# Optimization experiments

Hardware: AMD Instinct MI355X
Metric: run time of the kernel (lower is better)

The kernel has to match this reference:

```python
import math
import jax, jax.numpy as jnp
import numpy as np

B, L, D, H = 4, 1024, 1024, 16
HD = D // H  # head_dim = 64


def rel_pos_embed(seq_len: int, dim: int, padding_idx: int = 0) -> jnp.ndarray:
    """RelativeSinusoidalPositionalEmbedding for seq_len > origin_shift case:
    table regenerated with num_embeddings = 2*seq_len, origin_shift = seq_len,
    positions = arange(-L, L) + L selects the full table. Returns [2L, dim]."""
    num = 2 * seq_len
    half = dim // 2
    scale = math.log(10000.0) / (half - 1)
    freq = np.exp(np.arange(half, dtype=np.float32) * -scale)
    pos = np.arange(-num // 2, num // 2, dtype=np.float32)
    emb = pos[:, None] * freq[None, :]                      # [2L, half]
    emb = np.concatenate([np.sin(emb), np.cos(emb)], axis=1).astype(np.float32)
    emb[padding_idx] = 0.0
    return jnp.asarray(emb)


def _shift(BD):
    """Transformer-XL shift: [b,n,L,2L] -> [b,n,L,L] aligning relative positions."""
    b, n, l, _ = BD.shape
    zero_pad = jnp.zeros((b, n, l, 1), BD.dtype)
    BD = jnp.concatenate([BD, zero_pad], axis=-1).reshape(b, n, -1, l)  # [b,n,2L+1,L]
    BD = BD[:, :, : 2 * l].reshape(b, n, l, -1)                          # [b,n,L,2L]
    return BD[..., l:]                                                    # [b,n,L,L]


def setup_inputs() -> dict:
    key = jax.random.key(0)
    k0, k1, k2, k3 = jax.random.split(key, 4)
    x = jax.random.normal(k0, (B, L, D), jnp.float32)
    Wqv = jax.random.normal(k1, (D, 2 * D), jnp.float32) * (1.0 / math.sqrt(D))
    r_r_bias = jax.random.normal(k2, (H, HD), jnp.float32) * 0.1
    r_w_bias = jax.random.normal(k3, (H, HD), jnp.float32) * 0.1
    mask = jnp.ones((B, L), jnp.int32)
    return {"x": x, "Wqv": Wqv, "r_r_bias": r_r_bias, "r_w_bias": r_w_bias, "mask": mask}


def reference(x, Wqv, r_r_bias, r_w_bias, mask):
    b, l, d = x.shape
    pos = rel_pos_embed(l, HD)                               # [2L, HD] (detached buffer)
    qv = x @ Wqv                                             # [b, L, 2D]
    q, v = jnp.split(qv, 2, axis=-1)
    q = q.reshape(b, l, H, HD).transpose(0, 2, 1, 3)         # [b, H, L, HD]
    v = v.reshape(b, l, H, HD).transpose(0, 2, 1, 3)
    k = x.reshape(b, l, H, HD).transpose(0, 2, 1, 3)         # k_as_x=True: k is x reshaped

    rw_head_q = q + r_r_bias[None, :, None, :]
    AC = jnp.einsum('bnqd,bnkd->bnqk', rw_head_q, k)         # [b,H,L,L]
    D_ = jnp.einsum('nd,ld->nl', r_w_bias, pos)[None, :, None, :]  # [1,H,1,2L]
    B_ = jnp.einsum('bnqd,ld->bnql', q, pos)                 # [b,H,L,2L]
    BD = _shift(B_ + D_)                                     # [b,H,L,L]

    attn = AC + BD
    attn = jnp.where(mask[:, None, None, :] == 0, -jnp.inf, attn)
    attn = jax.nn.softmax(attn, axis=-1)                     # dropout is identity (eval)
    out = jnp.einsum('bnqk,bnkd->bnqd', attn, v)
    return out.transpose(0, 2, 1, 3).reshape(b, l, d)
```

## Files before the change

### kernel.cpp

```cpp
#include <hip/hip_runtime.h>
#include <hip/hip_bf16.h>
#include <math.h>


typedef __attribute__((ext_vector_type(8))) short short8;
typedef __attribute__((ext_vector_type(4))) short short4v;
typedef __attribute__((ext_vector_type(4))) float f32x4;

#define MFMA16(a,b,c) __builtin_amdgcn_mfma_f32_16x16x32_bf16(a,b,c,0,0,0)

__device__ __forceinline__ short f2bf(float f) {
  union { float f; unsigned int u; } v; v.f = f;
  unsigned int u = v.u;
  u += 0x7FFFu + ((u >> 16) & 1u);
  return (short)(u >> 16);
}
__device__ __forceinline__ float bf2f(short h) {
  union { unsigned int u; float f; } v;
  v.u = ((unsigned int)(unsigned short)h) << 16;
  return v.f;
}
__device__ __forceinline__ void glds16(const short* g, short* l) {
  __builtin_amdgcn_global_load_lds(
      (const __attribute__((address_space(1))) void*)g,
      (__attribute__((address_space(3))) void*)l, 16, 0, 0);
}

__global__ __launch_bounds__(256) void k_trig(float* __restrict__ T) {
  int idx = blockIdx.x * 256 + threadIdx.x;
  int l = idx >> 6, c = idx & 63, cc = c & 31;
  float fr = (float)exp(-(double)cc * 0.2971077539347156);
  double ang = (double)l * (double)fr;
  T[idx] = (float)((c < 32) ? sin(ang) : cos(ang));
}

__global__ __launch_bounds__(256) void k_split_x(const float* __restrict__ x,
    short* __restrict__ xh, short* __restrict__ xl) {
  int i = blockIdx.x * 256 + threadIdx.x;
  f32x4 v = ((const f32x4*)x)[i];
  short4v h, l;
#pragma unroll
  for (int c = 0; c < 4; ++c) {
    short hb = f2bf(v[c]);
    h[c] = hb;
    l[c] = f2bf(v[c] - bf2f(hb));
  }
  ((short4v*)xh)[i] = h;
  ((short4v*)xl)[i] = l;
}

__global__ __launch_bounds__(256) void k_wt(const float* __restrict__ W,
    short* __restrict__ wth, short* __restrict__ wtl) {
  __shared__ __align__(16) float tile[64*65];
  int n0 = blockIdx.x * 64, k0 = blockIdx.y * 64;
  int tid = threadIdx.x;
#pragma unroll
  for (int i = 0; i < 16; ++i) {
    int e = tid + i*256, r = e >> 6, c = e & 63;
    tile[r*65 + c] = W[(k0 + r)*2048 + n0 + c];
  }
  __syncthreads();
#pragma unroll
  for (int i = 0; i < 16; ++i) {
    int e = tid + i*256, r = e >> 6, c = e & 63;
    float v = tile[c*65 + r];
    short hb = f2bf(v);
    wth[(n0 + r)*1024 + k0 + c] = hb;
    wtl[(n0 + r)*1024 + k0 + c] = f2bf(v - bf2f(hb));
  }
}

__global__ __launch_bounds__(256) void k_gemm(
    const short* __restrict__ xh, const short* __restrict__ xl,
    const short* __restrict__ wth, const short* __restrict__ wtl,
    float* __restrict__ qf, short* __restrict__ vbt) {
  __shared__ __align__(16) short Ah[128*32], Al[128*32], Bh[128*32], Bl[128*32];
  int tid = threadIdx.x;
  int m0 = blockIdx.x * 128, n0 = blockIdx.y * 128;
  int lane = tid & 63, w = tid >> 6;
  int wm = w >> 1, wn = w & 1;
  int g = lane >> 4, lr = lane & 15;
  f32x4 acc[4][4] = {};
  for (int kt = 0; kt < 32; ++kt) {
    int k0 = kt * 32;
#pragma unroll
    for (int p = 0; p < 2; ++p) {
      int e = p*256 + tid;
      int r = e >> 2, c8 = (e & 3) * 8, e8 = e * 8;
      glds16(&xh [(m0+r)*1024 + k0 + c8], &Ah[e8]);
      glds16(&xl [(m0+r)*1024 + k0 + c8], &Al[e8]);
      glds16(&wth[(n0+r)*1024 + k0 + c8], &Bh[e8]);
      glds16(&wtl[(n0+r)*1024 + k0 + c8], &Bl[e8]);
    }
    __syncthreads();
    short8 ah[4], al[4], bh[4], bl[4];
#pragma unroll
    for (int mf = 0; mf < 4; ++mf) {
      int row = wm*64 + mf*16 + lr;
      ah[mf] = *(short8*)&Ah[row*32 + g*8];
      al[mf] = *(short8*)&Al[row*32 + g*8];
    }
#pragma unroll
    for (int nf = 0; nf < 4; ++nf) {
      int row = wn*64 + nf*16 + lr;
      bh[nf] = *(short8*)&Bh[row*32 + g*8];
      bl[nf] = *(short8*)&Bl[row*32 + g*8];
    }
    __builtin_amdgcn_s_setprio(1);
#pragma unroll
    for (int mf = 0; mf < 4; ++mf)
#pragma unroll
      for (int nf = 0; nf < 4; ++nf) {
        acc[mf][nf] = MFMA16(ah[mf], bh[nf], acc[mf][nf]);
        acc[mf][nf] = MFMA16(al[mf], bh[nf], acc[mf][nf]);
        acc[mf][nf] = MFMA16(ah[mf], bl[nf], acc[mf][nf]);
      }
    __builtin_amdgcn_s_setprio(0);
    __syncthreads();
  }
#pragma unroll
  for (int mf = 0; mf < 4; ++mf)
#pragma unroll
    for (int nf = 0; nf < 4; ++nf) {
      int row0 = m0 + wm*64 + mf*16 + g*4;
      int col  = n0 + wn*64 + nf*16 + lr;
      if (col < 1024) {
#pragma unroll
        for (int ri = 0; ri < 4; ++ri)
          qf[(row0 + ri)*1024 + col] = acc[mf][nf][ri];
      } else {
        int c2 = col - 1024, h = c2 >> 6, d = c2 & 63;
        int b = row0 >> 10, l0 = row0 & 1023;
        short4v pk;
#pragma unroll
        for (int ri = 0; ri < 4; ++ri) pk[ri] = f2bf(acc[mf][nf][ri]);
        *(short4v*)&vbt[((b*16 + h)*64 + d)*1024 + l0] = pk;
      }
    }
}

__global__ __launch_bounds__(256) void k_qcat(const float* __restrict__ qf,
    const float* __restrict__ rrb, const float* __restrict__ rwb,
    const float* __restrict__ T, short* __restrict__ qch, short* __restrict__ qcl) {
  int row = blockIdx.x * 4 + (threadIdx.x >> 6);
  int lane = threadIdx.x & 63;
  int b = row >> 14, h = (row >> 10) & 15, l = row & 1023;
  float q  = qf[(b*1024 + l)*1024 + h*64 + lane];
  float qa = q + rrb[h*64 + lane];
  float qb = q + rwb[h*64 + lane];
  int c = lane & 31;
  float qs = __shfl(qb, c, 64);
  float qc = __shfl(qb, c + 32, 64);
  float ts = T[l*64 + c];
  float tc = T[l*64 + c + 32];
  float v2 = (lane < 32) ? (qs*tc + qc*ts) : (qc*tc - qs*ts);
  short ha = f2bf(qa), h2 = f2bf(v2);
  qch[row*128 + lane]      = ha;
  qcl[row*128 + lane]      = f2bf(qa - bf2f(ha));
  qch[row*128 + 64 + lane] = h2;
  qcl[row*128 + 64 + lane] = f2bf(v2 - bf2f(h2));
}

__global__ __launch_bounds__(256) void k_kcat(const float* __restrict__ x,
    const float* __restrict__ T, short* __restrict__ kch, short* __restrict__ kcl) {
  int row = blockIdx.x * 4 + (threadIdx.x >> 6);
  int lane = threadIdx.x & 63;
  int b = row >> 14, h = (row >> 10) & 15, k = row & 1023;
  float xv = x[(b*1024 + k)*1024 + h*64 + lane];
  float tv = T[k*64 + lane];
  short hx = f2bf(xv), ht = f2bf(tv);
  int sw = k & 7;
  int c0 = lane, c1 = 64 + lane;
  int p0 = ((((c0 >> 3) ^ sw) << 3) | (c0 & 7));
  int p1 = ((((c1 >> 3) ^ sw) << 3) | (c1 & 7));
  kch[row*128 + p0] = hx;
  kcl[row*128 + p0] = f2bf(xv - bf2f(hx));
  kch[row*128 + p1] = ht;
  kcl[row*128 + p1] = f2bf(tv - bf2f(ht));
}

#define NKT 32
#define PLDW 40
__global__ __launch_bounds__(256, 2) void k_attn(
    const short* __restrict__ qch, const short* __restrict__ qcl,
    const short* __restrict__ kch, const short* __restrict__ kcl,
    const short* __restrict__ vbt, float* __restrict__ out) {
  __shared__ __align__(16) short Kh[2][32*128], Kl[2][32*128];
  __shared__ __align__(16) short Pl[4][2][16*PLDW];
  int tid = threadIdx.x, lane = tid & 63, w = tid >> 6;
  int g = lane >> 4, lr = lane & 15;
  int id = blockIdx.x;
  int s = id >> 3, xcd = id & 7;
  int bh = xcd*8 + (s & 7), qt = s >> 3;
  int q0 = qt * 128;
  short8 qh[2][4], ql[2][4];
#pragma unroll
  for (int m = 0; m < 2; ++m) {
    int qrow = bh*1024 + q0 + w*32 + m*16 + lr;
#pragma unroll
    for (int kc = 0; kc < 4; ++kc) {
      qh[m][kc] = *(const short8*)&qch[qrow*128 + kc*32 + g*8];
      ql[m][kc] = *(const short8*)&qcl[qrow*128 + kc*32 + g*8];
    }
  }
  f32x4 o[2][5] = {};
  float m_run[2][4];
#pragma unroll
  for (int m = 0; m < 2; ++m)
#pragma unroll
    for (int r = 0; r < 4; ++r) m_run[m][r] = -1e30f;
  short8 onesv;
#pragma unroll
  for (int i = 0; i < 8; ++i) onesv[i] = (short)0x3F80;
#pragma unroll
  for (int p = 0; p < 2; ++p) {
    int e8 = (p*256 + tid) * 8;
    glds16(&kch[(bh*1024)*128 + e8], &Kh[0][e8]);
    glds16(&kcl[(bh*1024)*128 + e8], &Kl[0][e8]);
  }
  __syncthreads();
  for (int kt = 0; kt < NKT; ++kt) {
    int cur = kt & 1;
    short8 vb[4];
#pragma unroll
    for (int df = 0; df < 4; ++df)
      vb[df] = *(const short8*)&vbt[(bh*64 + df*16 + lr)*1024 + kt*32 + g*8];
    if (kt + 1 < NKT) {
      int off = (bh*1024 + (kt+1)*32)*128;
#pragma unroll
      for (int p = 0; p < 2; ++p) {
        int e8 = (p*256 + tid) * 8;
        glds16(&kch[off + e8], &Kh[cur^1][e8]);
        glds16(&kcl[off + e8], &Kl[cur^1][e8]);
      }
    }
    f32x4 sacc[2][2] = {};
    __builtin_amdgcn_s_setprio(1);
#pragma unroll
    for (int kc = 0; kc < 4; ++kc)
#pragma unroll
      for (int nf = 0; nf < 2; ++nf) {
        int boff = (nf*16 + lr)*256 + ((((kc<<2) + g) ^ (lr & 7)) << 4);
        short8 kbh = *(short8*)((char*)&Kh[cur][0] + boff);
        short8 kbl = *(short8*)((char*)&Kl[cur][0] + boff);
#pragma unroll
        for (int m = 0; m < 2; ++m) {
          sacc[m][nf] = MFMA16(qh[m][kc], kbh, sacc[m][nf]);
          sacc[m][nf] = MFMA16(ql[m][kc], kbh, sacc[m][nf]);
          sacc[m][nf] = MFMA16(qh[m][kc], kbl, sacc[m][nf]);
        }
      }
    __builtin_amdgcn_s_setprio(0);
    float mt[2][4];
#pragma unroll
    for (int m = 0; m < 2; ++m)
#pragma unroll
      for (int r = 0; r < 4; ++r)
        mt[m][r] = fmaxf(sacc[m][0][r], sacc[m][1][r]);
#pragma unroll
    for (int off = 1; off < 16; off <<= 1)
#pragma unroll
      for (int m = 0; m < 2; ++m)
#pragma unroll
        for (int r = 0; r < 4; ++r)
          mt[m][r] = fmaxf(mt[m][r], __shfl_xor(mt[m][r], off, 64));
    float dmax = mt[0][0] - m_run[0][0];
#pragma unroll
    for (int m = 0; m < 2; ++m)
#pragma unroll
      for (int r = 0; r < 4; ++r)
        dmax = fmaxf(dmax, mt[m][r] - m_run[m][r]);
    if (!__all(dmax <= 8.0f)) {
#pragma unroll
      for (int m = 0; m < 2; ++m)
#pragma unroll
        for (int r = 0; r < 4; ++r) {
          float mn = fmaxf(m_run[m][r], mt[m][r]);
          float sc = __expf(m_run[m][r] - mn);
          m_run[m][r] = mn;
#pragma unroll
          for (int df = 0; df < 5; ++df) o[m][df][r] *= sc;
        }
    }
#pragma unroll
    for (int m = 0; m < 2; ++m)
#pragma unroll
      for (int nf = 0; nf < 2; ++nf)
#pragma unroll
        for (int r = 0; r < 4; ++r) {
          float p = __expf(sacc[m][nf][r] - m_run[m][r]);
          Pl[w][m][(g*4 + r)*PLDW + nf*16 + lr] = f2bf(p);
        }
    __builtin_amdgcn_s_setprio(1);
#pragma unroll
    for (int m = 0; m < 2; ++m) {
      short8 pa = *(short8*)&Pl[w][m][lr*PLDW + g*8];
#pragma unroll
      for (int df = 0; df < 4; ++df)
        o[m][df] = MFMA16(pa, vb[df], o[m][df]);
      o[m][4] = MFMA16(pa, onesv, o[m][4]);
    }
    __builtin_amdgcn_s_setprio(0);
    __syncthreads();
  }
  int b = bh >> 4, h = bh & 15;
#pragma unroll
  for (int m = 0; m < 2; ++m)
#pragma unroll
    for (int df = 0; df < 4; ++df)
#pragma unroll
      for (int r = 0; r < 4; ++r) {
        int qa = q0 + w*32 + m*16 + g*4 + r;
        out[(b*1024 + qa)*1024 + h*64 + df*16 + lr] = o[m][df][r] / o[m][4][r];
      }
}

extern "C" void kernel_launch(void* const* d_in, const int* in_sizes, int n_in,
                              void* d_out, int out_size, void* d_ws, size_t ws_size,
                              hipStream_t stream) {
  const float* x   = (const float*)d_in[0];
  const float* Wqv = (const float*)d_in[1];
  const float* rrb = (const float*)d_in[2];
  const float* rwb = (const float*)d_in[3];
  float* out = (float*)d_out;
  char* ws = (char*)d_ws;
  const size_t MB = 1u << 20;
  float* T   = (float*)(ws);
  short* vbt = (short*)(ws + 1*MB);
  short* qch = (short*)(ws + 9*MB);
  short* qcl = (short*)(ws + 25*MB);
  short* kch = (short*)(ws + 41*MB);
  short* kcl = (short*)(ws + 57*MB);
  short* xh  = (short*)(ws + 41*MB);
  short* xl  = (short*)(ws + 49*MB);
  short* wth = (short*)(ws + 57*MB);
  short* wtl = (short*)(ws + 61*MB);
  float* qf  = (float*)d_out;

  hipLaunchKernelGGL(k_trig,   dim3(256),      dim3(256), 0, stream, T);
  hipLaunchKernelGGL(k_split_x,dim3(4096),     dim3(256), 0, stream, x, xh, xl);
  hipLaunchKernelGGL(k_wt,     dim3(32, 16),   dim3(256), 0, stream, Wqv, wth, wtl);
  hipLaunchKernelGGL(k_gemm,   dim3(32, 16),   dim3(256), 0, stream, xh, xl, wth, wtl, qf, vbt);
  hipLaunchKernelGGL(k_qcat,   dim3(16384),    dim3(256), 0, stream, qf, rrb, rwb, T, qch, qcl);
  hipLaunchKernelGGL(k_kcat,   dim3(16384),    dim3(256), 0, stream, x, T, kch, kcl);
  hipLaunchKernelGGL(k_attn,   dim3(512),      dim3(256), 0, stream, qch, qcl, kch, kcl, vbt, out);
}
```

Before: 249.2 us.

## Split attention over key halves with combine kernel, double-buffer GEMM, trim V-block MFMAs

The attention kernel now splits the key range into two halves across twice as many blocks (1024 instead of 512) and targets four blocks per CU via launch bounds. A new combine kernel merges the unnormalized partial outputs using saved row max and sum. The goal is to fill more CUs and hide latency, at the cost of extra partial-output traffic and one more launch. Separately, the QV GEMM double-buffers its LDS tiles and drops the low-weight MFMA for V columns, which only need bf16 output. The online-softmax rescale check is also made cheaper: the cross-lane max reduction now runs only when some lane exceeds its threshold.

```diff
diff --git a/kernel.cpp b/kernel.cpp
--- a/kernel.cpp
+++ b/kernel.cpp
@@ -74,48 +74,71 @@
     const short* __restrict__ xh, const short* __restrict__ xl,
     const short* __restrict__ wth, const short* __restrict__ wtl,
     float* __restrict__ qf, short* __restrict__ vbt) {
-  __shared__ __align__(16) short Ah[128*32], Al[128*32], Bh[128*32], Bl[128*32];
+  __shared__ __align__(16) short Ah[2][128*32], Al[2][128*32],
+                                 Bh[2][128*32], Bl[2][128*32];
   int tid = threadIdx.x;
   int m0 = blockIdx.x * 128, n0 = blockIdx.y * 128;
+  bool vblock = (n0 >= 1024);
   int lane = tid & 63, w = tid >> 6;
   int wm = w >> 1, wn = w & 1;
   int g = lane >> 4, lr = lane & 15;
   f32x4 acc[4][4] = {};
+#define GSTAGE(kt, buf) do { \
+    int k0_ = (kt)*32; \
+    _Pragma("unroll") \
+    for (int p = 0; p < 2; ++p) { \
+      int e = p*256 + tid; \
+      int r = e >> 2, c8 = (e & 3)*8, e8 = e*8; \
+      glds16(&xh [(m0+r)*1024 + k0_ + c8], &Ah[buf][e8]); \
+      glds16(&xl [(m0+r)*1024 + k0_ + c8], &Al[buf][e8]); \
+      glds16(&wth[(n0+r)*1024 + k0_ + c8], &Bh[buf][e8]); \
+      if (!vblock) glds16(&wtl[(n0+r)*1024 + k0_ + c8], &Bl[buf][e8]); \
+    } \
+  } while (0)
+  GSTAGE(0, 0);
+  __syncthreads();
   for (int kt = 0; kt < 32; ++kt) {
-    int k0 = kt * 32;
-#pragma unroll
-    for (int p = 0; p < 2; ++p) {
-      int e = p*256 + tid;
-      int r = e >> 2, c8 = (e & 3) * 8, e8 = e * 8;
-      glds16(&xh [(m0+r)*1024 + k0 + c8], &Ah[e8]);
-      glds16(&xl [(m0+r)*1024 + k0 + c8], &Al[e8]);
-      glds16(&wth[(n0+r)*1024 + k0 + c8], &Bh[e8]);
-      glds16(&wtl[(n0+r)*1024 + k0 + c8], &Bl[e8]);
-    }
-    __syncthreads();
+    int cur = kt & 1;
+    if (kt + 1 < 32) GSTAGE(kt + 1, cur ^ 1);
     short8 ah[4], al[4], bh[4], bl[4];
 #pragma unroll
     for (int mf = 0; mf < 4; ++mf) {
       int row = wm*64 + mf*16 + lr;
-      ah[mf] = *(short8*)&Ah[row*32 + g*8];
-      al[mf] = *(short8*)&Al[row*32 + g*8];
+      ah[mf] = *(short8*)&Ah[cur][row*32 + g*8];
+      al[mf] = *(short8*)&Al[cur][row*32 + g*8];
     }
 #pragma unroll
     for (int nf = 0; nf < 4; ++nf) {
       int row = wn*64 + nf*16 + lr;
-      bh[nf] = *(short8*)&Bh[row*32 + g*8];
-      bl[nf] = *(short8*)&Bl[row*32 + g*8];
-    }
-    __builtin_amdgcn_s_setprio(1);
-#pragma unroll
-    for (int mf = 0; mf < 4; ++mf)
+      bh[nf] = *(short8*)&Bh[cur][row*32 + g*8];
+    }
+    if (!vblock) {
 #pragma unroll
       for (int nf = 0; nf < 4; ++nf) {
-        acc[mf][nf] = MFMA16(ah[mf], bh[nf], acc[mf][nf]);
-        acc[mf][nf] = MFMA16(al[mf], bh[nf], acc[mf][nf]);
-        acc[mf][nf] = MFMA16(ah[mf], bl[nf], acc[mf][nf]);
-      }
-    __builtin_amdgcn_s_setprio(0);
+        int row = wn*64 + nf*16 + lr;
+        bl[nf] = *(short8*)&Bl[cur][row*32 + g*8];
+      }
+      __builtin_amdgcn_s_setprio(1);
+#pragma unroll
+      for (int mf = 0; mf < 4; ++mf)
+#pragma unroll
+        for (int nf = 0; nf < 4; ++nf) {
+          acc[mf][nf] = MFMA16(ah[mf], bh[nf], acc[mf][nf]);
+          acc[mf][nf] = MFMA16(al[mf], bh[nf], acc[mf][nf]);
+          acc[mf][nf] = MFMA16(ah[mf], bl[nf], acc[mf][nf]);
+        }
+      __builtin_amdgcn_s_setprio(0);
+    } else {
+      __builtin_amdgcn_s_setprio(1);
+#pragma unroll
+      for (int mf = 0; mf < 4; ++mf)
+#pragma unroll
+        for (int nf = 0; nf < 4; ++nf) {
+          acc[mf][nf] = MFMA16(ah[mf], bh[nf], acc[mf][nf]);
+          acc[mf][nf] = MFMA16(al[mf], bh[nf], acc[mf][nf]);
+        }
+      __builtin_amdgcn_s_setprio(0);
+    }
     __syncthreads();
   }
 #pragma unroll
@@ -179,19 +202,20 @@
   kcl[row*128 + p1] = f2bf(tv - bf2f(ht));
 }
 
-#define NKT 32
+#define NKT 16
 #define PLDW 40
-__global__ __launch_bounds__(256, 2) void k_attn(
+__global__ __launch_bounds__(256, 4) void k_attn(
     const short* __restrict__ qch, const short* __restrict__ qcl,
     const short* __restrict__ kch, const short* __restrict__ kcl,
-    const short* __restrict__ vbt, float* __restrict__ out) {
+    const short* __restrict__ vbt, float* __restrict__ p0,
+    float* __restrict__ p1, float* __restrict__ ml) {
   __shared__ __align__(16) short Kh[2][32*128], Kl[2][32*128];
   __shared__ __align__(16) short Pl[4][2][16*PLDW];
   int tid = threadIdx.x, lane = tid & 63, w = tid >> 6;
   int g = lane >> 4, lr = lane & 15;
   int id = blockIdx.x;
   int s = id >> 3, xcd = id & 7;
-  int bh = xcd*8 + (s & 7), qt = s >> 3;
+  int bh = xcd*8 + (s & 7), qt = (s >> 3) & 7, sp = s >> 6;
   int q0 = qt * 128;
   short8 qh[2][4], ql[2][4];
 #pragma unroll
@@ -212,21 +236,25 @@
   short8 onesv;
 #pragma unroll
   for (int i = 0; i < 8; ++i) onesv[i] = (short)0x3F80;
-#pragma unroll
-  for (int p = 0; p < 2; ++p) {
-    int e8 = (p*256 + tid) * 8;
-    glds16(&kch[(bh*1024)*128 + e8], &Kh[0][e8]);
-    glds16(&kcl[(bh*1024)*128 + e8], &Kl[0][e8]);
+  {
+    int kbase = (bh*1024 + sp*512)*128;
+#pragma unroll
+    for (int p = 0; p < 2; ++p) {
+      int e8 = (p*256 + tid) * 8;
+      glds16(&kch[kbase + e8], &Kh[0][e8]);
+      glds16(&kcl[kbase + e8], &Kl[0][e8]);
+    }
   }
   __syncthreads();
-  for (int kt = 0; kt < NKT; ++kt) {
-    int cur = kt & 1;
+  for (int t = 0; t < NKT; ++t) {
+    int cur = t & 1;
+    int ktg = sp*16 + t;
     short8 vb[4];
 #pragma unroll
     for (int df = 0; df < 4; ++df)
-      vb[df] = *(const short8*)&vbt[(bh*64 + df*16 + lr)*1024 + kt*32 + g*8];
-    if (kt + 1 < NKT) {
-      int off = (bh*1024 + (kt+1)*32)*128;
+      vb[df] = *(const short8*)&vbt[(bh*64 + df*16 + lr)*1024 + ktg*32 + g*8];
+    if (t + 1 < NKT) {
+      int off = (bh*1024 + (ktg+1)*32)*128;
 #pragma unroll
       for (int p = 0; p < 2; ++p) {
         int e8 = (p*256 + tid) * 8;
@@ -251,31 +279,28 @@
         }
       }
     __builtin_amdgcn_s_setprio(0);
-    float mt[2][4];
+    float pm[2][4];
+    int trig = 0;
 #pragma unroll
     for (int m = 0; m < 2; ++m)
 #pragma unroll
-      for (int r = 0; r < 4; ++r)
-        mt[m][r] = fmaxf(sacc[m][0][r], sacc[m][1][r]);
-#pragma unroll
-    for (int off = 1; off < 16; off <<= 1)
+      for (int r = 0; r < 4; ++r) {
+        pm[m][r] = fmaxf(sacc[m][0][r], sacc[m][1][r]);
+        trig |= (pm[m][r] > m_run[m][r] + 8.0f);
+      }
+    if (__any(trig)) {
+#pragma unroll
+      for (int off = 1; off < 16; off <<= 1)
+#pragma unroll
+        for (int m = 0; m < 2; ++m)
+#pragma unroll
+          for (int r = 0; r < 4; ++r)
+            pm[m][r] = fmaxf(pm[m][r], __shfl_xor(pm[m][r], off, 64));
 #pragma unroll
       for (int m = 0; m < 2; ++m)
 #pragma unroll
-        for (int r = 0; r < 4; ++r)
-          mt[m][r] = fmaxf(mt[m][r], __shfl_xor(mt[m][r], off, 64));
-    float dmax = mt[0][0] - m_run[0][0];
-#pragma unroll
-    for (int m = 0; m < 2; ++m)
-#pragma unroll
-      for (int r = 0; r < 4; ++r)
-        dmax = fmaxf(dmax, mt[m][r] - m_run[m][r]);
-    if (!__all(dmax <= 8.0f)) {
-#pragma unroll
-      for (int m = 0; m < 2; ++m)
-#pragma unroll
         for (int r = 0; r < 4; ++r) {
-          float mn = fmaxf(m_run[m][r], mt[m][r]);
+          float mn = fmaxf(m_run[m][r], pm[m][r]);
           float sc = __expf(m_run[m][r] - mn);
           m_run[m][r] = mn;
 #pragma unroll
@@ -303,6 +328,7 @@
     __builtin_amdgcn_s_setprio(0);
     __syncthreads();
   }
+  float* pp = sp ? p1 : p0;
   int b = bh >> 4, h = bh & 15;
 #pragma unroll
   for (int m = 0; m < 2; ++m)
@@ -311,8 +337,37 @@
 #pragma unroll
       for (int r = 0; r < 4; ++r) {
         int qa = q0 + w*32 + m*16 + g*4 + r;
-        out[(b*1024 + qa)*1024 + h*64 + df*16 + lr] = o[m][df][r] / o[m][4][r];
-      }
+        pp[(b*1024 + qa)*1024 + h*64 + df*16 + lr] = o[m][df][r];
+      }
+  if (lr == 0) {
+#pragma unroll
+    for (int m = 0; m < 2; ++m)
+#pragma unroll
+      for (int r = 0; r < 4; ++r) {
+        int qa = q0 + w*32 + m*16 + g*4 + r;
+        int mlr = (sp*65536 + bh*1024 + qa)*2;
+        ml[mlr]     = m_run[m][r];
+        ml[mlr + 1] = o[m][4][r];
+      }
+  }
+}
+
+__global__ __launch_bounds__(256) void k_comb(const float* p0,
+    const float* __restrict__ p1, const float* __restrict__ ml, float* outp) {
+  int idx = (blockIdx.x*256 + threadIdx.x) * 4;
+  int b = idx >> 20, qa = (idx >> 10) & 1023, h = (idx >> 6) & 15;
+  int row = (b*16 + h)*1024 + qa;
+  float m0 = ml[row*2],            l0 = ml[row*2 + 1];
+  float m1 = ml[(65536 + row)*2],  l1 = ml[(65536 + row)*2 + 1];
+  float mm = fmaxf(m0, m1);
+  float w0 = __expf(m0 - mm), w1 = __expf(m1 - mm);
+  float inv = 1.0f / (l0*w0 + l1*w1);
+  f32x4 a = *(const f32x4*)&p0[idx];
+  f32x4 c = *(const f32x4*)&p1[idx];
+  f32x4 r;
+#pragma unroll
+  for (int i = 0; i < 4; ++i) r[i] = (a[i]*w0 + c[i]*w1) * inv;
+  *(f32x4*)&outp[idx] = r;
 }
 
 extern "C" void kernel_launch(void* const* d_in, const int* in_sizes, int n_in,
@@ -331,11 +386,14 @@
   short* qcl = (short*)(ws + 25*MB);
   short* kch = (short*)(ws + 41*MB);
   short* kcl = (short*)(ws + 57*MB);
+  float* p1  = (float*)(ws + 73*MB);
+  float* ml  = (float*)(ws + 89*MB);
   short* xh  = (short*)(ws + 41*MB);
   short* xl  = (short*)(ws + 49*MB);
   short* wth = (short*)(ws + 57*MB);
   short* wtl = (short*)(ws + 61*MB);
   float* qf  = (float*)d_out;
+  float* p0  = (float*)d_out;
 
   hipLaunchKernelGGL(k_trig,   dim3(256),      dim3(256), 0, stream, T);
   hipLaunchKernelGGL(k_split_x,dim3(4096),     dim3(256), 0, stream, x, xh, xl);
@@ -343,5 +401,6 @@
   hipLaunchKernelGGL(k_gemm,   dim3(32, 16),   dim3(256), 0, stream, xh, xl, wth, wtl, qf, vbt);
   hipLaunchKernelGGL(k_qcat,   dim3(16384),    dim3(256), 0, stream, qf, rrb, rwb, T, qch, qcl);
   hipLaunchKernelGGL(k_kcat,   dim3(16384),    dim3(256), 0, stream, x, T, kch, kcl);
-  hipLaunchKernelGGL(k_attn,   dim3(512),      dim3(256), 0, stream, qch, qcl, kch, kcl, vbt, out);
-}
+  hipLaunchKernelGGL(k_attn,   dim3(1024),     dim3(256), 0, stream, qch, qcl, kch, kcl, vbt, p0, p1, ml);
+  hipLaunchKernelGGL(k_comb,   dim3(4096),     dim3(256), 0, stream, p0, p1, ml, out);
+}
```

After: 268.8 us. +7.9%, slower.
